# Kernel optimization log

Measured on AMD Instinct MI355X. Metric: run time of the kernel, lower is better.

## Reference

```python
import jax, jax.numpy as jnp
import numpy as np

ALPHA = 1.5
BETA = 45.0
LAMDA = 0.5
B = 8192   # batch_size
D = 128    # feature dim (hardcoded in original via zeros((1,128)))
V = 4      # number of views stacked in fj
EPS = 1e-12  # F.normalize eps


def _l2norm_rows(x):
    n = jnp.sqrt(jnp.sum(x * x, axis=-1, keepdims=True))
    return x / jnp.maximum(n, EPS)


def setup_inputs() -> dict:
    key = jax.random.key(0)
    k1, k2 = jax.random.split(key)
    fi = jax.random.normal(k1, (B, D), dtype=jnp.float32)
    fj = jax.random.normal(k2, (V, B, D), dtype=jnp.float32)
    # L2-normalize embeddings so exp(beta*(SVM - lamda)) stays finite (beta=45)
    fi = _l2norm_rows(fi)
    fj = _l2norm_rows(fj)
    return {"fi": fi, "fj": fj, "b": V}


def avg_svm(fi, fj):
    # Original: per-row softmax-weighted average of fj rows, renormalized,
    # dotted with fi row, averaged over the batch.
    A = fi @ fj.T                      # [B, B] pairwise logits
    W = jax.nn.softmax(A, axis=1)      # softmax over j (alphalist / sumofalpha)
    Vw = W @ fj                        # [B, D] softmax-weighted averages
    Vn = _l2norm_rows(Vw)              # F.normalize(p=2, dim=1)
    return jnp.mean(jnp.sum(fi * Vn, axis=1))  # mean_i fi[i] . Vn[i]


def reference(fi, fj, b):
    b = int(b)
    # SMM1 is recomputed identically every outer iteration in the original;
    # compute once and multiply the per-iteration term by (b-1).
    smm1 = avg_svm(fi, fi)
    if b > 2:
        # inner loop: SMM2sum is a running (cumulative) sum over j=1..b-2,
        # and exp(beta*(SMM2sum - lamda)) is added at every step.
        s_vals = jnp.stack([avg_svm(fi, fj[j]) for j in range(1, b - 1)])
        cum = jnp.cumsum(s_vals)
        ssum = jnp.sum(jnp.exp(BETA * (cum - LAMDA)))
    else:
        ssum = jnp.exp(BETA * (avg_svm(fi, fj) - LAMDA))
    term = (1.0 / ALPHA) * jnp.log1p(jnp.exp(-ALPHA * (smm1 - LAMDA))) \
         + (1.0 / BETA) * jnp.log1p(ssum)
    loss = (b - 1) * term
    return jnp.squeeze(loss)
```

## Files before the change

kernel.cpp:

```cpp
#include <hip/hip_runtime.h>

#define BDIM 8192
#define DDIM 128

typedef __attribute__((ext_vector_type(4))) float floatx4;
typedef __attribute__((ext_vector_type(4))) int   intx4;
typedef __attribute__((ext_vector_type(8))) int   intx8;

#define SLAB (BDIM * DDIM)
#define G8_OFF 64
#define G8T_OFF (64 + 3 * SLAB)

__device__ inline void load_lds16(const void* g, void* l) {
    __builtin_amdgcn_global_load_lds(
        (const __attribute__((address_space(1))) unsigned int*)g,
        (__attribute__((address_space(3))) unsigned int*)l, 16, 0, 0);
}

__device__ inline intx8 ld_pair(const char* base, int c0) {
    union { intx8 v; intx4 h[2]; } u;
    u.h[0] = *(const intx4*)(base + c0 * 16);
    u.h[1] = *(const intx4*)(base + (c0 ^ 1) * 16);
    return u.v;
}

__device__ inline float exp_fast(float x) {
    return __builtin_amdgcn_exp2f(x * 1.44269504088896341f);
}

__global__ __launch_bounds__(256)
void prep_kernel(const float* __restrict__ fi, const float* __restrict__ fj,
                 unsigned char* __restrict__ g8, unsigned char* __restrict__ g8T,
                 float* __restrict__ acc)
{
    const int p = blockIdx.y;
    const int kblock = blockIdx.x;
    const int rbase = kblock * 32;
    const int tid = threadIdx.x;
    if (p == 0 && kblock == 0 && tid < 8) acc[tid] = 0.f;
    const float* src = (p == 0) ? fi : (fj + (size_t)p * SLAB);

    __shared__ __align__(16) unsigned char T8[32][144];

    {
        const int row = tid >> 3, c = tid & 7;
        const float* sp = src + (size_t)(rbase + row) * DDIM + c * 16;
        float4 f0 = ((const float4*)sp)[0];
        float4 f1 = ((const float4*)sp)[1];
        float4 f2 = ((const float4*)sp)[2];
        float4 f3 = ((const float4*)sp)[3];
        alignas(16) int w[4];
        w[0] = __builtin_amdgcn_cvt_pk_fp8_f32(f0.x, f0.y, 0, false);
        w[0] = __builtin_amdgcn_cvt_pk_fp8_f32(f0.z, f0.w, w[0], true);
        w[1] = __builtin_amdgcn_cvt_pk_fp8_f32(f1.x, f1.y, 0, false);
        w[1] = __builtin_amdgcn_cvt_pk_fp8_f32(f1.z, f1.w, w[1], true);
        w[2] = __builtin_amdgcn_cvt_pk_fp8_f32(f2.x, f2.y, 0, false);
        w[2] = __builtin_amdgcn_cvt_pk_fp8_f32(f2.z, f2.w, w[2], true);
        w[3] = __builtin_amdgcn_cvt_pk_fp8_f32(f3.x, f3.y, 0, false);
        w[3] = __builtin_amdgcn_cvt_pk_fp8_f32(f3.z, f3.w, w[3], true);
        int4 v = *(int4*)w;
        *(int4*)(g8 + (size_t)p * SLAB + (size_t)(rbase + row) * DDIM + c * 16) = v;
        *(int4*)(&T8[row][c * 16]) = v;
    }
    __syncthreads();
    {
        const int d = tid >> 1, half = tid & 1;
        alignas(16) unsigned char bb[16];
        #pragma unroll
        for (int i = 0; i < 16; ++i) bb[i] = T8[half * 16 + i][d];
        *(int4*)(g8T + (size_t)p * SLAB + (size_t)kblock * 4096 + d * 32 + half * 16) =
            *(int4*)bb;
    }
}

__global__ __launch_bounds__(256, 3)
void flash_kernel(const float* __restrict__ fi,
                  const unsigned char* __restrict__ g8,
                  const unsigned char* __restrict__ g8T,
                  float* __restrict__ acc)
{
    const int b = blockIdx.x;
    const int gp = (b & 7) * 96 + (b >> 3);
    const int p = gp >> 8;
    const int qbase = (gp & 255) * 32;
    const int tid = threadIdx.x;
    const int wave = tid >> 6, lane = tid & 63;
    const int quad = lane >> 4, col = lane & 15;

    __shared__ __align__(16) char smem[40960];
    #define KOFF 0
    #define VOFF 16384
    #define POFF 32768

    const unsigned char* g8p  = g8  + (size_t)p * SLAB;
    const unsigned char* g8Tp = g8T + (size_t)p * SLAB;

    intx8 qf[2];
    #pragma unroll
    for (int qt = 0; qt < 2; ++qt) {
        const intx4* qp = (const intx4*)(g8 + (size_t)(qbase + qt * 16 + col) * DDIM +
                                         quad * 32);
        union { intx8 v; intx4 h[2]; } u;
        u.h[0] = qp[0];
        u.h[1] = qp[1];
        qf[qt] = u.v;
    }

    floatx4 O[2][2];
    #pragma unroll
    for (int qt = 0; qt < 2; ++qt)
        #pragma unroll
        for (int j = 0; j < 2; ++j)
            O[qt][j] = (floatx4){0.f, 0.f, 0.f, 0.f};

    const unsigned char* gK[4];
    const unsigned char* gV[4];
    #pragma unroll
    for (int i = 0; i < 4; ++i) {
        int s = i * 64 + lane;
        int key = s >> 3, cp = s & 7;
        int c = cp ^ (key & 7);
        gK[i] = g8p + (size_t)(wave * 32 + key) * DDIM + c * 16;
        int t = wave * 256 + i * 64 + lane;
        int d = t >> 3, cq = t & 7;
        int cv = cq ^ (d & 7);
        gV[i] = g8Tp + (size_t)(cv >> 1) * 4096 + d * 32 + (cv & 1) * 16;
    }

    #pragma unroll
    for (int i = 0; i < 4; ++i) {
        load_lds16(gK[i], smem + KOFF + wave * 4096 + i * 1024);
        gK[i] += 16384;
    }
    #pragma unroll
    for (int i = 0; i < 4; ++i) {
        load_lds16(gV[i], smem + VOFF + wave * 4096 + i * 1024);
        gV[i] += 16384;
    }

    for (int k = 0; k < 64; ++k) {
        asm volatile("s_waitcnt vmcnt(4)" ::: "memory");

        floatx4 S[2][2];
        __builtin_amdgcn_s_setprio(1);
        #pragma unroll
        for (int kt = 0; kt < 2; ++kt) {
            const int key = kt * 16 + col;
            const int c0 = (quad * 2) ^ (key & 7);
            intx8 kf = ld_pair(smem + KOFF + wave * 4096 + key * 128, c0);
            #pragma unroll
            for (int qt = 0; qt < 2; ++qt)
                S[kt][qt] = __builtin_amdgcn_mfma_scale_f32_16x16x128_f8f6f4(
                    kf, qf[qt], (floatx4){0.f, 0.f, 0.f, 0.f},
                    0, 0, 0, 127, 0, 127);
        }
        __builtin_amdgcn_s_setprio(0);

        asm volatile("s_waitcnt lgkmcnt(0)" ::: "memory");
        if (k < 63) {
            #pragma unroll
            for (int i = 0; i < 4; ++i) {
                load_lds16(gK[i], smem + KOFF + wave * 4096 + i * 1024);
                gK[i] += 16384;
            }
        }

        char* pw = smem + POFF + ((k & 1) << 12);
        #pragma unroll
        for (int kt = 0; kt < 2; ++kt)
            #pragma unroll
            for (int qt = 0; qt < 2; ++qt) {
                int v = __builtin_amdgcn_cvt_pk_fp8_f32(
                    exp_fast(S[kt][qt][0]), exp_fast(S[kt][qt][1]), 0, false);
                v = __builtin_amdgcn_cvt_pk_fp8_f32(
                    exp_fast(S[kt][qt][2]), exp_fast(S[kt][qt][3]), v, true);
                const int q = qt * 16 + col;
                *(int*)(pw + q * 128 +
                        (((wave * 2 + kt) ^ (q & 7)) << 4) + quad * 4) = v;
            }

        asm volatile("s_waitcnt lgkmcnt(0)\n\ts_barrier" ::: "memory");

        asm volatile("s_waitcnt vmcnt(4)" ::: "memory");

        __builtin_amdgcn_s_setprio(1);
        {
            const char* pr = smem + POFF + ((k & 1) << 12);
            intx8 vf[2];
            #pragma unroll
            for (int j = 0; j < 2; ++j) {
                const int d = (wave * 2 + j) * 16 + col;
                vf[j] = ld_pair(smem + VOFF + d * 128, (quad * 2) ^ (d & 7));
            }
            #pragma unroll
            for (int qt = 0; qt < 2; ++qt) {
                const int q = qt * 16 + col;
                intx8 pf = ld_pair(pr + q * 128, (quad * 2) ^ (q & 7));
                #pragma unroll
                for (int j = 0; j < 2; ++j)
                    O[qt][j] = __builtin_amdgcn_mfma_scale_f32_16x16x128_f8f6f4(
                        pf, vf[j], O[qt][j], 0, 0, 0, 127, 0, 127);
            }
        }
        __builtin_amdgcn_s_setprio(0);

        asm volatile("s_waitcnt lgkmcnt(0)" ::: "memory");
        if (k < 63) {
            #pragma unroll
            for (int i = 0; i < 4; ++i) {
                load_lds16(gV[i], smem + VOFF + wave * 4096 + i * 1024);
                gV[i] += 16384;
            }
        }
    }

    float* pdot = (float*)(smem + POFF);
    float* pnrm = (float*)(smem + POFF + 512);
    #pragma unroll
    for (int qt = 0; qt < 2; ++qt)
        #pragma unroll
        for (int r = 0; r < 4; ++r) {
            const int q = qt * 16 + quad * 4 + r;
            float dot = 0.f, nr = 0.f;
            #pragma unroll
            for (int j = 0; j < 2; ++j) {
                float o = O[qt][j][r];
                float fq = fi[(size_t)(qbase + q) * DDIM + (wave * 2 + j) * 16 + col];
                dot += fq * o;
                nr += o * o;
            }
            #pragma unroll
            for (int m = 1; m < 16; m <<= 1) {
                dot += __shfl_xor(dot, m, 64);
                nr  += __shfl_xor(nr,  m, 64);
            }
            if (col == 0) {
                pdot[wave * 32 + q] = dot;
                pnrm[wave * 32 + q] = nr;
            }
        }
    __syncthreads();
    if (tid < 32) {
        const int q = tid;
        float D = pdot[q] + pdot[32 + q] + pdot[64 + q] + pdot[96 + q];
        float N = pnrm[q] + pnrm[32 + q] + pnrm[64 + q] + pnrm[96 + q];
        float val = D * rsqrtf(fmaxf(N, 1e-30f));
        #pragma unroll
        for (int m = 1; m < 32; m <<= 1) val += __shfl_xor(val, m, 64);
        if (tid == 0) atomicAdd(&acc[p], val);
    }
}

__global__ void final_kernel(const float* __restrict__ acc, float* __restrict__ out)
{
    if (threadIdx.x == 0 && blockIdx.x == 0) {
        const double s0 = (double)acc[0] / (double)BDIM;
        const double s1 = (double)acc[1] / (double)BDIM;
        const double s2 = (double)acc[2] / (double)BDIM;
        const double t1 = (1.0 / 1.5) * log1p(exp(-1.5 * (s0 - 0.5)));
        const double ssum = exp(45.0 * (s1 - 0.5)) + exp(45.0 * (s1 + s2 - 0.5));
        const double t2 = (1.0 / 45.0) * log1p(ssum);
        out[0] = (float)(3.0 * (t1 + t2));
    }
}

extern "C" void kernel_launch(void* const* d_in, const int* in_sizes, int n_in,
                              void* d_out, int out_size, void* d_ws, size_t ws_size,
                              hipStream_t stream)
{
    const float* fi = (const float*)d_in[0];
    const float* fj = (const float*)d_in[1];

    float* acc = (float*)d_ws;
    unsigned char* g8  = (unsigned char*)d_ws + G8_OFF;
    unsigned char* g8T = (unsigned char*)d_ws + G8T_OFF;

    prep_kernel <<<dim3(BDIM / 32, 3), 256, 0, stream>>>(fi, fj, g8, g8T, acc);
    flash_kernel<<<dim3(768), 256, 0, stream>>>(fi, g8, g8T, acc);
    final_kernel<<<1, 64, 0, stream>>>(acc, (float*)d_out);
}
```

Before: 154.8 us.

## Load K/V fragments directly from global into registers, dropping LDS staging

Replaces the global-to-LDS async loads of K and V tiles, and the swizzled LDS reads that followed, with direct 32-byte per-lane global loads into registers. These are double-buffered across two unrolled half-iterations. LDS shrinks to only the P exchange buffer, which could allow more blocks per CU and removes LDS traffic and waits. The cost is more register pressure, and global loads that are less coalesced and rely on cache, possibly with latency exposed by compiler-inserted vmcnt waits.

Result: slower. 189.3 us (+22.3%).

```diff
diff --git a/kernel.cpp b/kernel.cpp
--- a/kernel.cpp
+++ b/kernel.cpp
@@ -10,12 +10,6 @@
 #define SLAB (BDIM * DDIM)
 #define G8_OFF 64
 #define G8T_OFF (64 + 3 * SLAB)
-
-__device__ inline void load_lds16(const void* g, void* l) {
-    __builtin_amdgcn_global_load_lds(
-        (const __attribute__((address_space(1))) unsigned int*)g,
-        (__attribute__((address_space(3))) unsigned int*)l, 16, 0, 0);
-}
 
 __device__ inline intx8 ld_pair(const char* base, int c0) {
     union { intx8 v; intx4 h[2]; } u;
@@ -87,10 +81,8 @@
     const int wave = tid >> 6, lane = tid & 63;
     const int quad = lane >> 4, col = lane & 15;
 
-    __shared__ __align__(16) char smem[40960];
-    #define KOFF 0
-    #define VOFF 16384
-    #define POFF 32768
+    __shared__ __align__(16) char smem[8192];
+    #define POFF 0
 
     const unsigned char* g8p  = g8  + (size_t)p * SLAB;
     const unsigned char* g8Tp = g8T + (size_t)p * SLAB;
@@ -113,57 +105,33 @@
         for (int j = 0; j < 2; ++j)
             O[qt][j] = (floatx4){0.f, 0.f, 0.f, 0.f};
 
-    const unsigned char* gK[4];
-    const unsigned char* gV[4];
-    #pragma unroll
-    for (int i = 0; i < 4; ++i) {
-        int s = i * 64 + lane;
-        int key = s >> 3, cp = s & 7;
-        int c = cp ^ (key & 7);
-        gK[i] = g8p + (size_t)(wave * 32 + key) * DDIM + c * 16;
-        int t = wave * 256 + i * 64 + lane;
-        int d = t >> 3, cq = t & 7;
-        int cv = cq ^ (d & 7);
-        gV[i] = g8Tp + (size_t)(cv >> 1) * 4096 + d * 32 + (cv & 1) * 16;
-    }
-
-    #pragma unroll
-    for (int i = 0; i < 4; ++i) {
-        load_lds16(gK[i], smem + KOFF + wave * 4096 + i * 1024);
-        gK[i] += 16384;
-    }
-    #pragma unroll
-    for (int i = 0; i < 4; ++i) {
-        load_lds16(gV[i], smem + VOFF + wave * 4096 + i * 1024);
-        gV[i] += 16384;
-    }
-
-    for (int k = 0; k < 64; ++k) {
-        asm volatile("s_waitcnt vmcnt(4)" ::: "memory");
-
+    const unsigned char* pK0 = g8p + (size_t)(wave * 32 + col) * DDIM + quad * 32;
+    const unsigned char* pK1 = pK0 + 16 * DDIM;
+    const unsigned char* pV0 = g8Tp + (size_t)quad * 4096 +
+                               (size_t)(wave * 2 * 16 + col) * 32;
+    const unsigned char* pV1 = pV0 + 16 * 32;
+
+    intx8 kA0, kA1, vA0, vA1, kB0, kB1, vB0, vB1;
+
+#define LOADT(K0, K1, V0, V1)                                          \
+    do {                                                               \
+        K0 = *(const intx8*)pK0; K1 = *(const intx8*)pK1;              \
+        V0 = *(const intx8*)pV0; V1 = *(const intx8*)pV1;              \
+        pK0 += 16384; pK1 += 16384; pV0 += 16384; pV1 += 16384;        \
+    } while (0)
+
+    auto half_iter = [&](int k, intx8 kf0, intx8 kf1, intx8 vf0, intx8 vf1) {
         floatx4 S[2][2];
         __builtin_amdgcn_s_setprio(1);
-        #pragma unroll
-        for (int kt = 0; kt < 2; ++kt) {
-            const int key = kt * 16 + col;
-            const int c0 = (quad * 2) ^ (key & 7);
-            intx8 kf = ld_pair(smem + KOFF + wave * 4096 + key * 128, c0);
-            #pragma unroll
-            for (int qt = 0; qt < 2; ++qt)
-                S[kt][qt] = __builtin_amdgcn_mfma_scale_f32_16x16x128_f8f6f4(
-                    kf, qf[qt], (floatx4){0.f, 0.f, 0.f, 0.f},
-                    0, 0, 0, 127, 0, 127);
-        }
+        S[0][0] = __builtin_amdgcn_mfma_scale_f32_16x16x128_f8f6f4(
+            kf0, qf[0], (floatx4){0.f, 0.f, 0.f, 0.f}, 0, 0, 0, 127, 0, 127);
+        S[0][1] = __builtin_amdgcn_mfma_scale_f32_16x16x128_f8f6f4(
+            kf0, qf[1], (floatx4){0.f, 0.f, 0.f, 0.f}, 0, 0, 0, 127, 0, 127);
+        S[1][0] = __builtin_amdgcn_mfma_scale_f32_16x16x128_f8f6f4(
+            kf1, qf[0], (floatx4){0.f, 0.f, 0.f, 0.f}, 0, 0, 0, 127, 0, 127);
+        S[1][1] = __builtin_amdgcn_mfma_scale_f32_16x16x128_f8f6f4(
+            kf1, qf[1], (floatx4){0.f, 0.f, 0.f, 0.f}, 0, 0, 0, 127, 0, 127);
         __builtin_amdgcn_s_setprio(0);
-
-        asm volatile("s_waitcnt lgkmcnt(0)" ::: "memory");
-        if (k < 63) {
-            #pragma unroll
-            for (int i = 0; i < 4; ++i) {
-                load_lds16(gK[i], smem + KOFF + wave * 4096 + i * 1024);
-                gK[i] += 16384;
-            }
-        }
 
         char* pw = smem + POFF + ((k & 1) << 12);
         #pragma unroll
@@ -181,37 +149,27 @@
 
         asm volatile("s_waitcnt lgkmcnt(0)\n\ts_barrier" ::: "memory");
 
-        asm volatile("s_waitcnt vmcnt(4)" ::: "memory");
-
+        const char* pr = smem + POFF + ((k & 1) << 12);
         __builtin_amdgcn_s_setprio(1);
-        {
-            const char* pr = smem + POFF + ((k & 1) << 12);
-            intx8 vf[2];
-            #pragma unroll
-            for (int j = 0; j < 2; ++j) {
-                const int d = (wave * 2 + j) * 16 + col;
-                vf[j] = ld_pair(smem + VOFF + d * 128, (quad * 2) ^ (d & 7));
-            }
-            #pragma unroll
-            for (int qt = 0; qt < 2; ++qt) {
-                const int q = qt * 16 + col;
-                intx8 pf = ld_pair(pr + q * 128, (quad * 2) ^ (q & 7));
-                #pragma unroll
-                for (int j = 0; j < 2; ++j)
-                    O[qt][j] = __builtin_amdgcn_mfma_scale_f32_16x16x128_f8f6f4(
-                        pf, vf[j], O[qt][j], 0, 0, 0, 127, 0, 127);
-            }
+        #pragma unroll
+        for (int qt = 0; qt < 2; ++qt) {
+            const int q = qt * 16 + col;
+            intx8 pf = ld_pair(pr + q * 128, (quad * 2) ^ (q & 7));
+            O[qt][0] = __builtin_amdgcn_mfma_scale_f32_16x16x128_f8f6f4(
+                pf, vf0, O[qt][0], 0, 0, 0, 127, 0, 127);
+            O[qt][1] = __builtin_amdgcn_mfma_scale_f32_16x16x128_f8f6f4(
+                pf, vf1, O[qt][1], 0, 0, 0, 127, 0, 127);
         }
         __builtin_amdgcn_s_setprio(0);
-
-        asm volatile("s_waitcnt lgkmcnt(0)" ::: "memory");
-        if (k < 63) {
-            #pragma unroll
-            for (int i = 0; i < 4; ++i) {
-                load_lds16(gV[i], smem + VOFF + wave * 4096 + i * 1024);
-                gV[i] += 16384;
-            }
-        }
+    };
+
+    LOADT(kA0, kA1, vA0, vA1);
+
+    for (int k = 0; k < 64; k += 2) {
+        LOADT(kB0, kB1, vB0, vB1);
+        half_iter(k, kA0, kA1, vA0, vA1);
+        if (k + 2 < 64) LOADT(kA0, kA1, vA0, vA1);
+        half_iter(k + 1, kB0, kB1, vB0, vB1);
     }
 
     float* pdot = (float*)(smem + POFF);
```

## Software-pipeline QK and PV MFMAs across iterations with one barrier per step

Applied to the files above, without the earlier changes.

Restructures the main loop into a prologue, a steady state and an epilogue. Each iteration now issues the QK^T MFMAs for tile k together with the PV MFMAs for tile k-1, using the P buffer written in the previous iteration. This removes one barrier per iteration and lets the exponent/convert work overlap with matrix ops. In exchange, waits become vmcnt(0), which drains all outstanding loads, and register pressure rises from holding more fragments live at once.

New measurement: 152.5 us. About the same (-1.5%).

```diff
diff --git a/kernel.cpp b/kernel.cpp
--- a/kernel.cpp
+++ b/kernel.cpp
@@ -127,45 +127,32 @@
         gV[i] = g8Tp + (size_t)(cv >> 1) * 4096 + d * 32 + (cv & 1) * 16;
     }
 
-    #pragma unroll
-    for (int i = 0; i < 4; ++i) {
-        load_lds16(gK[i], smem + KOFF + wave * 4096 + i * 1024);
-        gK[i] += 16384;
-    }
-    #pragma unroll
-    for (int i = 0; i < 4; ++i) {
-        load_lds16(gV[i], smem + VOFF + wave * 4096 + i * 1024);
-        gV[i] += 16384;
-    }
-
-    for (int k = 0; k < 64; ++k) {
-        asm volatile("s_waitcnt vmcnt(4)" ::: "memory");
-
-        floatx4 S[2][2];
-        __builtin_amdgcn_s_setprio(1);
-        #pragma unroll
-        for (int kt = 0; kt < 2; ++kt) {
-            const int key = kt * 16 + col;
-            const int c0 = (quad * 2) ^ (key & 7);
-            intx8 kf = ld_pair(smem + KOFF + wave * 4096 + key * 128, c0);
-            #pragma unroll
-            for (int qt = 0; qt < 2; ++qt)
-                S[kt][qt] = __builtin_amdgcn_mfma_scale_f32_16x16x128_f8f6f4(
-                    kf, qf[qt], (floatx4){0.f, 0.f, 0.f, 0.f},
-                    0, 0, 0, 127, 0, 127);
+    auto stageK = [&]() {
+        #pragma unroll
+        for (int i = 0; i < 4; ++i) {
+            load_lds16(gK[i], smem + KOFF + wave * 4096 + i * 1024);
+            gK[i] += 16384;
         }
-        __builtin_amdgcn_s_setprio(0);
-
-        asm volatile("s_waitcnt lgkmcnt(0)" ::: "memory");
-        if (k < 63) {
-            #pragma unroll
-            for (int i = 0; i < 4; ++i) {
-                load_lds16(gK[i], smem + KOFF + wave * 4096 + i * 1024);
-                gK[i] += 16384;
-            }
+    };
+    auto stageV = [&]() {
+        #pragma unroll
+        for (int i = 0; i < 4; ++i) {
+            load_lds16(gV[i], smem + VOFF + wave * 4096 + i * 1024);
+            gV[i] += 16384;
         }
-
-        char* pw = smem + POFF + ((k & 1) << 12);
+    };
+
+    const char* kb0 = smem + KOFF + wave * 4096 + (col) * 128;
+    const char* kb1 = smem + KOFF + wave * 4096 + (16 + col) * 128;
+    const int   kc  = (quad * 2) ^ (col & 7);
+    const char* vb0 = smem + VOFF + ((wave * 2 + 0) * 16 + col) * 128;
+    const char* vb1 = smem + VOFF + ((wave * 2 + 1) * 16 + col) * 128;
+    const int   vc0 = (quad * 2) ^ (((wave * 2 + 0) * 16 + col) & 7);
+    const int   vc1 = (quad * 2) ^ (((wave * 2 + 1) * 16 + col) & 7);
+    const int   pq0 = col, pq1 = 16 + col;
+
+    auto expP = [&](floatx4 S[2][2], int par) {
+        char* pw = smem + POFF + (par << 12);
         #pragma unroll
         for (int kt = 0; kt < 2; ++kt)
             #pragma unroll
@@ -178,40 +165,86 @@
                 *(int*)(pw + q * 128 +
                         (((wave * 2 + kt) ^ (q & 7)) << 4) + quad * 4) = v;
             }
-
+    };
+
+    stageK();
+    asm volatile("s_waitcnt vmcnt(0)" ::: "memory");
+    {
+        floatx4 S[2][2];
+        intx8 kf0 = ld_pair(kb0, kc);
+        intx8 kf1 = ld_pair(kb1, kc);
+        __builtin_amdgcn_s_setprio(1);
+        S[0][0] = __builtin_amdgcn_mfma_scale_f32_16x16x128_f8f6f4(
+            kf0, qf[0], (floatx4){0.f,0.f,0.f,0.f}, 0, 0, 0, 127, 0, 127);
+        S[0][1] = __builtin_amdgcn_mfma_scale_f32_16x16x128_f8f6f4(
+            kf0, qf[1], (floatx4){0.f,0.f,0.f,0.f}, 0, 0, 0, 127, 0, 127);
+        S[1][0] = __builtin_amdgcn_mfma_scale_f32_16x16x128_f8f6f4(
+            kf1, qf[0], (floatx4){0.f,0.f,0.f,0.f}, 0, 0, 0, 127, 0, 127);
+        S[1][1] = __builtin_amdgcn_mfma_scale_f32_16x16x128_f8f6f4(
+            kf1, qf[1], (floatx4){0.f,0.f,0.f,0.f}, 0, 0, 0, 127, 0, 127);
+        __builtin_amdgcn_s_setprio(0);
+        asm volatile("s_waitcnt lgkmcnt(0)" ::: "memory");
+        stageK();
+        stageV();
+        expP(S, 0);
         asm volatile("s_waitcnt lgkmcnt(0)\n\ts_barrier" ::: "memory");
-
-        asm volatile("s_waitcnt vmcnt(4)" ::: "memory");
-
+    }
+
+    for (int k = 1; k < 64; ++k) {
+        asm volatile("s_waitcnt vmcnt(0)" ::: "memory");
+
+        intx8 kf0 = ld_pair(kb0, kc);
+        intx8 kf1 = ld_pair(kb1, kc);
+        intx8 vf0 = ld_pair(vb0, vc0);
+        intx8 vf1 = ld_pair(vb1, vc1);
+        const char* pr = smem + POFF + (((k - 1) & 1) << 12);
+        intx8 pf0 = ld_pair(pr + pq0 * 128, (quad * 2) ^ (pq0 & 7));
+        intx8 pf1 = ld_pair(pr + pq1 * 128, (quad * 2) ^ (pq1 & 7));
+
+        floatx4 S[2][2];
         __builtin_amdgcn_s_setprio(1);
-        {
-            const char* pr = smem + POFF + ((k & 1) << 12);
-            intx8 vf[2];
-            #pragma unroll
-            for (int j = 0; j < 2; ++j) {
-                const int d = (wave * 2 + j) * 16 + col;
-                vf[j] = ld_pair(smem + VOFF + d * 128, (quad * 2) ^ (d & 7));
-            }
-            #pragma unroll
-            for (int qt = 0; qt < 2; ++qt) {
-                const int q = qt * 16 + col;
-                intx8 pf = ld_pair(pr + q * 128, (quad * 2) ^ (q & 7));
-                #pragma unroll
-                for (int j = 0; j < 2; ++j)
-                    O[qt][j] = __builtin_amdgcn_mfma_scale_f32_16x16x128_f8f6f4(
-                        pf, vf[j], O[qt][j], 0, 0, 0, 127, 0, 127);
-            }
-        }
+        S[0][0] = __builtin_amdgcn_mfma_scale_f32_16x16x128_f8f6f4(
+            kf0, qf[0], (floatx4){0.f,0.f,0.f,0.f}, 0, 0, 0, 127, 0, 127);
+        S[0][1] = __builtin_amdgcn_mfma_scale_f32_16x16x128_f8f6f4(
+            kf0, qf[1], (floatx4){0.f,0.f,0.f,0.f}, 0, 0, 0, 127, 0, 127);
+        S[1][0] = __builtin_amdgcn_mfma_scale_f32_16x16x128_f8f6f4(
+            kf1, qf[0], (floatx4){0.f,0.f,0.f,0.f}, 0, 0, 0, 127, 0, 127);
+        S[1][1] = __builtin_amdgcn_mfma_scale_f32_16x16x128_f8f6f4(
+            kf1, qf[1], (floatx4){0.f,0.f,0.f,0.f}, 0, 0, 0, 127, 0, 127);
+        O[0][0] = __builtin_amdgcn_mfma_scale_f32_16x16x128_f8f6f4(
+            pf0, vf0, O[0][0], 0, 0, 0, 127, 0, 127);
+        O[0][1] = __builtin_amdgcn_mfma_scale_f32_16x16x128_f8f6f4(
+            pf0, vf1, O[0][1], 0, 0, 0, 127, 0, 127);
+        O[1][0] = __builtin_amdgcn_mfma_scale_f32_16x16x128_f8f6f4(
+            pf1, vf0, O[1][0], 0, 0, 0, 127, 0, 127);
+        O[1][1] = __builtin_amdgcn_mfma_scale_f32_16x16x128_f8f6f4(
+            pf1, vf1, O[1][1], 0, 0, 0, 127, 0, 127);
         __builtin_amdgcn_s_setprio(0);
 
         asm volatile("s_waitcnt lgkmcnt(0)" ::: "memory");
-        if (k < 63) {
-            #pragma unroll
-            for (int i = 0; i < 4; ++i) {
-                load_lds16(gV[i], smem + VOFF + wave * 4096 + i * 1024);
-                gV[i] += 16384;
-            }
-        }
+        if (k < 63) stageK();
+        stageV();
+
+        expP(S, k & 1);
+
+        asm volatile("s_waitcnt lgkmcnt(0)\n\ts_barrier" ::: "memory");
+    }
+
+    asm volatile("s_waitcnt vmcnt(0)" ::: "memory");
+    {
+        intx8 vf0 = ld_pair(vb0, vc0);
+        intx8 vf1 = ld_pair(vb1, vc1);
+        const char* pr = smem + POFF + ((63 & 1) << 12);
+        intx8 pf0 = ld_pair(pr + pq0 * 128, (quad * 2) ^ (pq0 & 7));
+        intx8 pf1 = ld_pair(pr + pq1 * 128, (quad * 2) ^ (pq1 & 7));
+        O[0][0] = __builtin_amdgcn_mfma_scale_f32_16x16x128_f8f6f4(
+            pf0, vf0, O[0][0], 0, 0, 0, 127, 0, 127);
+        O[0][1] = __builtin_amdgcn_mfma_scale_f32_16x16x128_f8f6f4(
+            pf0, vf1, O[0][1], 0, 0, 0, 127, 0, 127);
+        O[1][0] = __builtin_amdgcn_mfma_scale_f32_16x16x128_f8f6f4(
+            pf1, vf0, O[1][0], 0, 0, 0, 127, 0, 127);
+        O[1][1] = __builtin_amdgcn_mfma_scale_f32_16x16x128_f8f6f4(
+            pf1, vf1, O[1][1], 0, 0, 0, 127, 0, 127);
     }
 
     float* pdot = (float*)(smem + POFF);
```
